# Performance work log

Measured on AMD Instinct MI355X. Metric: run time of the kernel, lower is better.

## Reference

```python
import math
import jax, jax.numpy as jnp
import numpy as np

Bn, NA, NE = 16384, 15, 16
H, NH, DH = 256, 4, 64
DO, DA, DE = 30, 32, 32
NACT, BS = 6, 2048


def setup_inputs():
    key = jax.random.key(0)
    c = [0]
    def nxt():
        c[0] += 1
        return jax.random.fold_in(key, c[0])
    def nrm(shape, scale=1.0):
        return jax.random.normal(nxt(), shape, jnp.float32) * scale
    sH = 1.0 / math.sqrt(H)
    own_raw = nrm((Bn, 1, DO))
    ally_raw = nrm((Bn, NA, DA))
    enemy_raw = nrm((Bn, NE, DE))
    # zero-rows encode invisible entities (mask is derived from all-zero check)
    mA = jax.random.bernoulli(nxt(), 0.8, (Bn, NA)).at[:, 0].set(True)
    mE = jax.random.bernoulli(nxt(), 0.8, (Bn, NE)).at[:, 0].set(True)
    ally_raw = ally_raw * mA[..., None]
    enemy_raw = enemy_raw * mE[..., None]
    return dict(
        own_raw=own_raw, ally_raw=ally_raw, enemy_raw=enemy_raw,
        hidden_state=nrm((Bn, H), 0.1),
        W_own=nrm((H, DO), 1.0 / math.sqrt(DO)), b_own=jnp.zeros((H,)),
        W_ally=nrm((H, DA), 1.0 / math.sqrt(DA)), b_ally=jnp.zeros((H,)),
        W_enemy=nrm((H, DE), 1.0 / math.sqrt(DE)), b_enemy=jnp.zeros((H,)),
        gt_w=nrm((2,), 0.1), gt_b=jnp.zeros((2,)),
        attnA_W=nrm((4, H, H), sH), attnA_b=jnp.zeros((4, H)),
        attnE_W=nrm((4, H, H), sH), attnE_b=jnp.zeros((4, H)),
        clnA_W=nrm((2, H, H), 0.1 * sH), clnA_b=jnp.zeros((2, H)),
        clnE_W=nrm((2, H, H), 0.1 * sH), clnE_b=jnp.zeros((2, H)),
        ln3_g=jnp.ones((3 * H,)), ln3_b=jnp.zeros((3 * H,)),
        gru_Wih=nrm((3 * H, 3 * H), 1.0 / math.sqrt(3 * H)),
        gru_Whh=nrm((3 * H, H), sH),
        gru_bih=jnp.zeros((3 * H,)), gru_bhh=jnp.zeros((3 * H,)),
        Wv_head=nrm((1, H), sH), bv_head=jnp.zeros((1,)),
        Wtb=nrm((2, H), sH), btb=jnp.zeros((2,)),
        log_tau=jnp.zeros((2,)),
        Wmq=nrm((H, H), sH), bmq=jnp.zeros((H,)),
        prototypes=nrm((NACT, H), sH),
        Wqs=nrm((H, H), sH), bqs=jnp.zeros((H,)),
        Wke=nrm((H, H), sH), bke=jnp.zeros((H,)),
        bs=BS,
    )


def _group_temp(cnt, w, b):
    # GroupTemp: positive temperature from group cardinality
    return jax.nn.softplus(w * jnp.log1p(cnt) + b) + 1.0


def _mhga(q, K, mask, temp, W, b):
    # multi-head group attention: single query over a small entity set
    B, N, _ = K.shape
    qh = (q @ W[0].T + b[0]).reshape(B, NH, DH)
    kh = (K @ W[1].T + b[1]).reshape(B, N, NH, DH)
    vh = (K @ W[2].T + b[2]).reshape(B, N, NH, DH)
    s = jnp.einsum('bhd,bnhd->bhn', qh, kh) / math.sqrt(DH)
    s = s / temp[:, None, None]
    s = jnp.where(mask[:, None, :], s, -1e30)
    p = jax.nn.softmax(s, axis=-1)
    z = jnp.einsum('bhn,bnhd->bhd', p, vh).reshape(B, H)
    return z @ W[3].T + b[3]


def _cln(x, cond, W, b, eps=1e-5):
    # conditional LayerNorm: scale/shift predicted from own-feature embedding
    mu = x.mean(-1, keepdims=True)
    var = ((x - mu) ** 2).mean(-1, keepdims=True)
    xn = (x - mu) * jax.lax.rsqrt(var + eps)
    gamma = 1.0 + cond @ W[0].T + b[0]
    beta = cond @ W[1].T + b[1]
    return gamma * xn + beta


def _ln(x, g, b, eps=1e-5):
    mu = x.mean(-1, keepdims=True)
    var = ((x - mu) ** 2).mean(-1, keepdims=True)
    return (x - mu) * jax.lax.rsqrt(var + eps) * g + b


def reference(own_raw, ally_raw, enemy_raw, hidden_state, W_own, b_own,
              W_ally, b_ally, W_enemy, b_enemy, gt_w, gt_b,
              attnA_W, attnA_b, attnE_W, attnE_b,
              clnA_W, clnA_b, clnE_W, clnE_b, ln3_g, ln3_b,
              gru_Wih, gru_Whh, gru_bih, gru_bhh,
              Wv_head, bv_head, Wtb, btb, log_tau,
              Wmq, bmq, prototypes, Wqs, bqs, Wke, bke, bs):
    ally_mask = jnp.any(ally_raw != 0, axis=-1)     # [B,nA]
    enemy_mask = jnp.any(enemy_raw != 0, axis=-1)   # [B,nE]
    e_own = own_raw @ W_own.T + b_own               # [B,1,H]
    A = ally_raw @ W_ally.T + b_ally                # [B,nA,H]
    E = enemy_raw @ W_enemy.T + b_enemy             # [B,nE,H]
    q_src = e_own[:, 0]
    tA = _group_temp(ally_mask.sum(-1).astype(jnp.float32), gt_w[0], gt_b[0])
    tE = _group_temp(enemy_mask.sum(-1).astype(jnp.float32), gt_w[1], gt_b[1])
    zA = _cln(_mhga(q_src, A, ally_mask, tA, attnA_W, attnA_b), q_src, clnA_W, clnA_b)
    zE = _cln(_mhga(q_src, E, enemy_mask, tE, attnE_W, attnE_b), q_src, clnE_W, clnE_b)
    u = _ln(jnp.concatenate([q_src, zA, zE], axis=-1), ln3_g, ln3_b)
    # GRUCell (PyTorch gate layout: r, z, n)
    gi = u @ gru_Wih.T + gru_bih
    gh = hidden_state @ gru_Whh.T + gru_bhh
    ir, iz, inn = jnp.split(gi, 3, axis=-1)
    hr, hz, hn = jnp.split(gh, 3, axis=-1)
    r = jax.nn.sigmoid(ir + hr)
    zg = jax.nn.sigmoid(iz + hz)
    n = jnp.tanh(inn + r * hn)
    h = (1.0 - zg) * n + zg * hidden_state
    V = h @ Wv_head.T + bv_head                     # [B,1]
    tb = h @ Wtb.T + btb
    b_move, b_shoot = tb[:, 0:1], tb[:, 1:2]
    tau_move = jnp.exp(log_tau[0]) + 1e-6
    tau_shoot = jnp.exp(log_tau[1]) + 1e-6
    # prototype movement head
    q_mv = h @ Wmq.T + bmq
    A_move = q_mv @ prototypes.T / math.sqrt(H)
    A_move = A_move - A_move.mean(-1, keepdims=True)
    Q_move = V + b_move + A_move / tau_move
    # shoot pointer head over enemies
    q_sh = h @ Wqs.T + bqs
    Ke = E @ Wke.T + bke
    a = jnp.einsum('bh,bnh->bn', q_sh, Ke) / math.sqrt(H)
    emf = enemy_mask.astype(a.dtype)
    den = jnp.maximum(emf.sum(1, keepdims=True), 1.0)
    a = a - (a * emf).sum(1, keepdims=True) / den
    a = jnp.where(enemy_mask, a, -1e30)
    Q_shoot = V + b_shoot + a / tau_shoot
    Q = jnp.concatenate([Q_move, Q_shoot], axis=-1)[:, None, :]  # [B,1,NACT+nE]
    return Q, h.reshape(bs, -1, H)
```

## Files before the change

kernel.cpp:

```cpp
#include <hip/hip_runtime.h>
#include <math.h>

#define BN 16384

typedef float f32x4 __attribute__((ext_vector_type(4)));
typedef short bf16x8v __attribute__((ext_vector_type(8)));
typedef unsigned short u16x8 __attribute__((ext_vector_type(8)));
typedef unsigned short u16x4 __attribute__((ext_vector_type(4)));

static __device__ inline unsigned short f2bf(float f) {
  unsigned u = __float_as_uint(f);
  return (unsigned short)((u + 0x8000u) >> 16);
}
static __device__ inline float bf2f(unsigned short u) {
  return __uint_as_float(((unsigned)u) << 16);
}

#define XS(r) (((r) >> 1) & 3)

#define WKA_OFF   0
#define WVA_OFF   8192
#define WKE_OFF   16384
#define WVE_OFF   24576
#define WKEF_OFF  32768
#define BKA_OFF   40960
#define BVA_OFF   41216
#define BKE_OFF   41472
#define BVE_OFF   41728
#define BKEF_OFF  41984
#define WMP_OFF   43008
#define BMP_OFF   44544
#define G_OFF     45056
#define BG_OFF    53248
#define WQB_OFF   53312
#define SC0_OFF   53568
#define BMG_OFF   53632
#define CLB_OFF   53888
#define BPJA_OFF  57088
#define BPJE_OFF  57344
#define BGRU_OFF  57600
#define BHD_OFF   16384

#define QSRC_OFF  65536
#define BUF1_OFF  (QSRC_OFF + BN*256)
#define BUF2_OFF  (BUF1_OFF + BN*256)
#define BUF3_OFF  (BUF2_OFF + BN*256)
#define BUF4_OFF  (BUF3_OFF + BN*256)
#define BUF5_OFF  (BUF4_OFF + BN*256)

#define GBUF_OFF  BUF1_OFF
#define AOUTA_OFF BUF3_OFF
#define AOUTE_OFF BUF4_OFF
#define GBB_OFF   BUF5_OFF
#define UB_OFF    (BUF5_OFF + 8388608)

#define HOFF      (BN*22)

#define MGB_S 0
#define CLA_S 65536
#define CLE_S 196608
#define PJA_S 327680
#define PJE_S 360448

__global__ __launch_bounds__(256) void k_fuseA(
    const float* __restrict__ attnA_W, const float* __restrict__ attnA_b,
    const float* __restrict__ attnE_W, const float* __restrict__ attnE_b,
    const float* __restrict__ W_ally,  const float* __restrict__ b_ally,
    const float* __restrict__ W_enemy, const float* __restrict__ b_enemy,
    const float* __restrict__ Wke,     const float* __restrict__ bke,
    const float* __restrict__ clnA_W,  const float* __restrict__ clnE_W,
    float* __restrict__ FW, unsigned short* __restrict__ WBc) {
  int g = blockIdx.x * 256 + threadIdx.x;
  if (g < 81920) {
    int u = g >> 1, t = g & 1;
    int m = u >> 13;
    int r = u & 8191;
    int d = r >> 5, j = r & 31;
    const float *Wout, *Win, *bin, *bout; float *dst, *dstb;
    switch (m) {
      case 0: Wout = attnA_W + 65536;  Win = W_ally;  bin = b_ally;  bout = attnA_b + 256; dst = FW + WKA_OFF;  dstb = FW + BKA_OFF;  break;
      case 1: Wout = attnA_W + 131072; Win = W_ally;  bin = b_ally;  bout = attnA_b + 512; dst = FW + WVA_OFF;  dstb = FW + BVA_OFF;  break;
      case 2: Wout = attnE_W + 65536;  Win = W_enemy; bin = b_enemy; bout = attnE_b + 256; dst = FW + WKE_OFF;  dstb = FW + BKE_OFF;  break;
      case 3: Wout = attnE_W + 131072; Win = W_enemy; bin = b_enemy; bout = attnE_b + 512; dst = FW + WVE_OFF;  dstb = FW + BVE_OFF;  break;
      default:Wout = Wke;              Win = W_enemy; bin = b_enemy; bout = bke;           dst = FW + WKEF_OFF; dstb = FW + BKEF_OFF; break;
    }
    const int c0 = t * 128;
    float acc = 0.f;
    for (int c = c0; c < c0 + 128; ++c) acc += Wout[d*256 + c] * Win[c*32 + j];
    acc += __shfl_xor(acc, 1);
    if (t == 0) dst[d*32 + j] = acc;
    if (j == 0) {
      float b = 0.f;
      for (int c = c0; c < c0 + 128; ++c) b += Wout[d*256 + c] * bin[c];
      b += __shfl_xor(b, 1);
      if (t == 0) dstb[d] = b + bout[d];
    }
  } else {
    int t = g - 81920;
    if (t < 65536) {
      int e = t * 4;
      const float* src = (e < 131072) ? clnA_W : clnE_W;
      int off = (e < 131072) ? 0 : 131072;
      float4 v = *(const float4*)(src + (e - off));
      u16x4 b; b.x = f2bf(v.x); b.y = f2bf(v.y); b.z = f2bf(v.z); b.w = f2bf(v.w);
      *(u16x4*)&WBc[CLA_S + e] = b;
    }
  }
}

__global__ __launch_bounds__(256) void k_fuseB(
    const float* __restrict__ protos, const float* __restrict__ Wmq,
    const float* __restrict__ bmq,    const float* __restrict__ Wqs,
    const float* __restrict__ bqs,
    const float* __restrict__ attnA_W, const float* __restrict__ attnA_b,
    const float* __restrict__ attnE_W, const float* __restrict__ attnE_b,
    const float* __restrict__ clnA_b,  const float* __restrict__ clnE_b,
    float* __restrict__ FW, unsigned short* __restrict__ WBc) {
  int g = blockIdx.x * 256 + threadIdx.x;
  const float* WKe_f = FW + WKEF_OFF;
  const float* bKe_f = FW + BKEF_OFF;
  if (g < 20480) {
    int u = g >> 1, tt = g & 1;
    const int c0 = tt * 128;
    if (u < 1536) {
      int i = u >> 8, c = u & 255;
      float acc = 0.f;
      for (int d = c0; d < c0 + 128; ++d) acc += protos[i*256 + d] * Wmq[d*256 + c];
      acc += __shfl_xor(acc, 1);
      if (tt == 0) FW[WMP_OFF + i*256 + c] = acc;
    } else if (u < 9728) {
      int r = u - 1536;
      int j = r >> 8, c = r & 255;
      float acc = 0.f;
      for (int d = c0; d < c0 + 128; ++d) acc += WKe_f[d*32 + j] * Wqs[d*256 + c];
      acc += __shfl_xor(acc, 1);
      if (tt == 0) FW[G_OFF + j*256 + c] = acc;
    } else if (u < 9984) {
      int c = u - 9728;
      float acc = 0.f;
      for (int d = c0; d < c0 + 128; ++d) acc += Wqs[d*256 + c] * bKe_f[d];
      acc += __shfl_xor(acc, 1);
      if (tt == 0) FW[WQB_OFF + c] = acc;
    } else if (u < 9990) {
      int i = u - 9984;
      float acc = 0.f;
      for (int d = c0; d < c0 + 128; ++d) acc += protos[i*256 + d] * bmq[d];
      acc += __shfl_xor(acc, 1);
      if (tt == 0) FW[BMP_OFF + i] = acc;
    } else if (u < 10022) {
      int j = u - 9990;
      float acc = 0.f;
      for (int d = c0; d < c0 + 128; ++d) acc += WKe_f[d*32 + j] * bqs[d];
      acc += __shfl_xor(acc, 1);
      if (tt == 0) FW[BG_OFF + j] = acc;
    } else if (u == 10022) {
      float acc = 0.f;
      for (int d = c0; d < c0 + 128; ++d) acc += bqs[d] * bKe_f[d];
      acc += __shfl_xor(acc, 1);
      if (tt == 0) FW[SC0_OFF] = acc;
    }
  } else if (g < 87296) {
    int t = g - 20480;
    if (t < 65536) {
      int r = t >> 8, c = t & 255;
      int br = r >> 7, jj = r & 127, h = jj >> 5, jc = jj & 31;
      const float* W0 = br ? attnE_W : attnA_W;
      const float* Wk = FW + (br ? WKE_OFF : WKA_OFF);
      float acc = 0.f;
      for (int d = 0; d < 64; ++d)
        acc += W0[(h*64+d)*256 + c] * Wk[(h*64+d)*32 + jc];
      WBc[MGB_S + r*256 + c] = f2bf(acc);
    } else if (t < 65792) {
      int r = t - 65536;
      int br = r >> 7, jj = r & 127, h = jj >> 5, jc = jj & 31;
      const float* b0 = br ? attnE_b : attnA_b;
      const float* Wk = FW + (br ? WKE_OFF : WKA_OFF);
      float acc = 0.f;
      for (int d = 0; d < 64; ++d) acc += b0[h*64+d] * Wk[(h*64+d)*32 + jc];
      FW[BMG_OFF + r] = acc;
    } else {
      int c = t - 65792;
      FW[CLB_OFF + c] = (c < 512) ? clnA_b[c] : clnE_b[c - 512];
    }
  } else {
    int t = g - 87296;
    if (t < 65536) {
      int br = t >> 15;
      int r0 = t & 32767;
      int o = r0 >> 7, r = r0 & 127, h = r >> 5, j = r & 31;
      const float* Wp = (br ? attnE_W : attnA_W) + 196608;
      const float* Wv = FW + (br ? WVE_OFF : WVA_OFF);
      float acc = 0.f;
      for (int d = 0; d < 64; ++d)
        acc += Wp[o*256 + h*64 + d] * Wv[(h*64+d)*32 + j];
      WBc[(br ? PJE_S : PJA_S) + o*128 + r] = f2bf(acc);
    } else if (t < 66048) {
      int r0 = t - 65536;
      int br = r0 >> 8, c = r0 & 255;
      const float* Wp = (br ? attnE_W : attnA_W) + 196608;
      const float* bv = FW + (br ? BVE_OFF : BVA_OFF);
      const float* pb = (br ? attnE_b : attnA_b) + 768;
      float acc = pb[c];
      for (int d = 0; d < 256; ++d) acc += Wp[c*256 + d] * bv[d];
      FW[(br ? BPJE_OFF : BPJA_OFF) + c] = acc;
    }
  }
}

__global__ __launch_bounds__(256) void k_fuse4(
    const float* __restrict__ Wv_head, const float* __restrict__ bv_head,
    const float* __restrict__ Wtb, const float* __restrict__ btb,
    float* __restrict__ FW, unsigned short* __restrict__ WHD) {
  int g = blockIdx.x * 256 + threadIdx.x;
  if (g < 32768) {
    int r = g >> 8, c = g & 255;
    float v;
    if (r == 0)       v = Wv_head[c];
    else if (r == 1)  v = Wtb[c];
    else if (r == 2)  v = Wtb[256 + c];
    else if (r < 9)   v = FW[WMP_OFF + (r - 3) * 256 + c];
    else if (r < 41)  v = FW[G_OFF + (r - 9) * 256 + c];
    else if (r == 41) v = FW[WQB_OFF + c];
    else              v = 0.f;
    WHD[r * 256 + c] = f2bf(v);
  } else if (g < 32896) {
    int r = g - 32768;
    float v;
    if (r == 0)       v = bv_head[0];
    else if (r == 1)  v = btb[0];
    else if (r == 2)  v = btb[1];
    else if (r < 9)   v = FW[BMP_OFF + r - 3];
    else if (r < 41)  v = FW[BG_OFF + r - 9];
    else if (r == 41) v = FW[SC0_OFF];
    else              v = 0.f;
    FW[BHD_OFF + r] = v;
  }
}

__global__ __launch_bounds__(256) void k_gruw2(
    const float* __restrict__ Wih, const float* __restrict__ Whh,
    const float* __restrict__ bih, const float* __restrict__ bhh,
    unsigned short* __restrict__ WF, float* __restrict__ BG) {
  int t = blockIdx.x * 256 + threadIdx.x;
  if (t < 131072) {
    int l = t & 63;
    int n = (t >> 6) & 3;
    int cq = (t >> 8) & 3;
    int bx = (t >> 10) & 3;
    int ch = t >> 12;
    int lr = l & 15, lk = l >> 4;
    int d = bx * 64 + cq * 16 + lr;
    int kb = ch * 32 + lk * 8;
    float fa[8];
    bool zero = (kb < 768) ? (n == 3) : (n == 2);
    if (zero) {
      #pragma unroll
      for (int i = 0; i < 8; ++i) fa[i] = 0.f;
    } else if (kb < 768) {
      const float* src = Wih + (long)(n * 256 + d) * 768 + kb;
      *(float4*)&fa[0] = *(const float4*)(src);
      *(float4*)&fa[4] = *(const float4*)(src + 4);
    } else {
      int rh = (n == 3 ? 512 : n * 256) + d;
      const float* src = Whh + (long)rh * 256 + (kb - 768);
      *(float4*)&fa[0] = *(const float4*)(src);
      *(float4*)&fa[4] = *(const float4*)(src + 4);
    }
    u16x8 pk;
    #pragma unroll
    for (int i = 0; i < 8; ++i) pk[i] = f2bf(fa[i]);
    *(u16x8*)&WF[(long)t * 8] = pk;
  } else if (t < 132096) {
    int p = t - 131072;
    int X = p >> 8, df = (p >> 6) & 3, g = (p >> 4) & 3, i = p & 15;
    int d = X * 64 + df * 16 + i;
    float v;
    if (g == 0)      v = bih[d] + bhh[d];
    else if (g == 1) v = bih[256 + d] + bhh[256 + d];
    else if (g == 2) v = bih[512 + d];
    else             v = bhh[512 + d];
    BG[p] = v;
  }
}

template<int K, int NOUT>
__global__ __launch_bounds__(256) void k_densek(
    const float* __restrict__ A, const float* __restrict__ W,
    const float* __restrict__ bias, unsigned short* __restrict__ Cb) {
  constexpr int KB = 32;
  __shared__ float As[64][36];
  const int tid = threadIdx.x;
  const int s0 = blockIdx.x * 64;
  const int o0 = blockIdx.y * 64;
  const int ox = (tid & 15) * 4;
  const int sy = (tid >> 4) * 4;
  float acc[4][4] = {};
  const float* Abase = A + (long)s0 * K;
  for (int idx = tid; idx < 64 * KB; idx += 256) {
    int s = idx >> 5, c = idx & 31;
    As[s][c] = (c < K) ? Abase[(long)s * K + c] : 0.f;
  }
  __syncthreads();
  for (int kk = 0; kk < KB; kk += 4) {
    float a4[4][4];
    #pragma unroll
    for (int sj = 0; sj < 4; ++sj)
      *(float4*)a4[sj] = *(const float4*)&As[sy + sj][kk];
    #pragma unroll
    for (int oi = 0; oi < 4; ++oi) {
      float w4[4];
      #pragma unroll
      for (int kx = 0; kx < 4; ++kx) {
        int k = kk + kx;
        w4[kx] = (k < K) ? W[(long)(o0 + ox + oi) * K + k] : 0.f;
      }
      #pragma unroll
      for (int sj = 0; sj < 4; ++sj)
        #pragma unroll
        for (int kx = 0; kx < 4; ++kx)
          acc[sj][oi] = fmaf(a4[sj][kx], w4[kx], acc[sj][oi]);
    }
  }
  #pragma unroll
  for (int sj = 0; sj < 4; ++sj) {
    u16x4 b4;
    b4.x = f2bf(acc[sj][0] + bias[o0 + ox + 0]);
    b4.y = f2bf(acc[sj][1] + bias[o0 + ox + 1]);
    b4.z = f2bf(acc[sj][2] + bias[o0 + ox + 2]);
    b4.w = f2bf(acc[sj][3] + bias[o0 + ox + 3]);
    *(u16x4*)&Cb[(long)(s0 + sy + sj) * NOUT + o0 + ox] = b4;
  }
}

#define MM_PROLOG(GDX)                                                        \
  __shared__ __align__(16) unsigned short As[4096];                           \
  __shared__ __align__(16) unsigned short Ws[4096];                           \
  const int tid = threadIdx.x;                                                \
  const int pid = blockIdx.y * (GDX) + blockIdx.x;                            \
  const int bx = (pid >> 3) % (GDX);                                          \
  const int by = ((pid >> 3) / (GDX)) * 8 + (pid & 7);                        \
  const long s0 = (long)by * 128;                                             \
  const int wv = tid >> 6, l = tid & 63;                                      \
  const int wm = (wv >> 1) * 64, wn = (wv & 1) * 64;                          \
  const int lr = l & 15, lk = l >> 4;                                         \
  const int wrow = tid >> 2;                                                  \
  const int wslot = tid & 3;                                                  \
  (void)wrow; (void)wslot;                                                    \
  f32x4 acc[4][4] = {};

#define MM_MFMA_STEP                                                          \
  {                                                                           \
    bf16x8v af[4], bw[4];                                                     \
    _Pragma("unroll")                                                         \
    for (int m = 0; m < 4; ++m) {                                             \
      const int r = wm + m * 16 + lr;                                         \
      af[m] = *(const bf16x8v*)&As[r * 32 + ((lk ^ XS(r)) * 8)];              \
    }                                                                         \
    _Pragma("unroll")                                                         \
    for (int n = 0; n < 4; ++n) {                                             \
      const int r = wn + n * 16 + lr;                                         \
      bw[n] = *(const bf16x8v*)&Ws[r * 32 + ((lk ^ XS(r)) * 8)];              \
    }                                                                         \
    _Pragma("unroll")                                                         \
    for (int m = 0; m < 4; ++m)                                               \
      _Pragma("unroll")                                                       \
      for (int n = 0; n < 4; ++n)                                             \
        acc[m][n] = __builtin_amdgcn_mfma_f32_16x16x32_bf16(af[m], bw[n], acc[m][n], 0, 0, 0); \
  }

__global__ __launch_bounds__(256) void k_mm_qs(
    const unsigned short* __restrict__ Abf, const unsigned short* __restrict__ W,
    const float* __restrict__ bias, unsigned short* __restrict__ Cg,
    unsigned short* __restrict__ Cgb) {
  MM_PROLOG(10)
  const int o0 = bx * 128;
  u16x8 pw[2], pa_b[2];
  const unsigned short* Wb = W + (long)o0 * 256;
  #pragma unroll
  for (int p = 0; p < 2; ++p) {
    const int r = wrow + 64 * p;
    pw[p]   = *(const u16x8*)(Wb + (long)r * 256 + wslot * 8);
    pa_b[p] = *(const u16x8*)(Abf + (s0 + r) * 256 + wslot * 8);
  }
  for (int ch = 0; ch < 8; ++ch) {
    if (ch) __syncthreads();
    #pragma unroll
    for (int p = 0; p < 2; ++p) {
      const int r = wrow + 64 * p;
      const int ps = (wslot ^ XS(r)) * 8;
      *(u16x8*)&Ws[r * 32 + ps] = pw[p];
      *(u16x8*)&As[r * 32 + ps] = pa_b[p];
    }
    __syncthreads();
    if (ch + 1 < 8) {
      const int k0 = (ch + 1) * 32;
      #pragma unroll
      for (int p = 0; p < 2; ++p) {
        const int r = wrow + 64 * p;
        pw[p]   = *(const u16x8*)(Wb + (long)r * 256 + k0 + wslot * 8);
        pa_b[p] = *(const u16x8*)(Abf + (s0 + r) * 256 + k0 + wslot * 8);
      }
    }
    MM_MFMA_STEP
  }
  if (bx < 2) {
    const int ob = bx * 128;
    #pragma unroll
    for (int n = 0; n < 4; ++n) {
      const float b = bias[o0 + wn + n * 16 + lr];
      #pragma unroll
      for (int m = 0; m < 4; ++m) {
        const long rowb = s0 + wm + m * 16 + lk * 4;
        #pragma unroll
        for (int r = 0; r < 4; ++r)
          Cg[(rowb + r) * 256 + ob + wn + n * 16 + lr] = f2bf(acc[m][n][r] + b);
      }
    }
  } else {
    const int ob = (bx - 2) * 128;
    #pragma unroll
    for (int n = 0; n < 4; ++n) {
      const float b = bias[o0 + wn + n * 16 + lr];
      #pragma unroll
      for (int m = 0; m < 4; ++m) {
        const long rowb = s0 + wm + m * 16 + lk * 4;
        #pragma unroll
        for (int r = 0; r < 4; ++r)
          Cgb[(rowb + r) * 1024 + ob + wn + n * 16 + lr] = f2bf(acc[m][n][r] + b);
      }
    }
  }
}

__global__ __launch_bounds__(256) void k_mm_pv(
    const unsigned short* __restrict__ pal, const unsigned short* __restrict__ W,
    const float* __restrict__ bias, unsigned short* __restrict__ CA,
    unsigned short* __restrict__ CE) {
  MM_PROLOG(4)
  const int o0 = bx * 128;
  const int br = bx >> 1;
  const unsigned short* Abf = pal + br * 128;
  u16x8 pw[2], pa_b[2];
  const unsigned short* Wb = W + (long)o0 * 128;
  #pragma unroll
  for (int p = 0; p < 2; ++p) {
    const int r = wrow + 64 * p;
    pw[p]   = *(const u16x8*)(Wb + (long)r * 128 + wslot * 8);
    pa_b[p] = *(const u16x8*)(Abf + (s0 + r) * 256 + wslot * 8);
  }
  for (int ch = 0; ch < 4; ++ch) {
    if (ch) __syncthreads();
    #pragma unroll
    for (int p = 0; p < 2; ++p) {
      const int r = wrow + 64 * p;
      const int ps = (wslot ^ XS(r)) * 8;
      *(u16x8*)&Ws[r * 32 + ps] = pw[p];
      *(u16x8*)&As[r * 32 + ps] = pa_b[p];
    }
    __syncthreads();
    if (ch + 1 < 4) {
      const int k0 = (ch + 1) * 32;
      #pragma unroll
      for (int p = 0; p < 2; ++p) {
        const int r = wrow + 64 * p;
        pw[p]   = *(const u16x8*)(Wb + (long)r * 128 + k0 + wslot * 8);
        pa_b[p] = *(const u16x8*)(Abf + (s0 + r) * 256 + k0 + wslot * 8);
      }
    }
    MM_MFMA_STEP
  }
  unsigned short* C = br ? CE : CA;
  const int ob = (bx & 1) * 128;
  #pragma unroll
  for (int n = 0; n < 4; ++n) {
    const float b = bias[o0 + wn + n * 16 + lr];
    #pragma unroll
    for (int m = 0; m < 4; ++m) {
      const long rowb = s0 + wm + m * 16 + lk * 4;
      #pragma unroll
      for (int r = 0; r < 4; ++r)
        C[(rowb + r) * 256 + ob + wn + n * 16 + lr] = f2bf(acc[m][n][r] + b);
    }
  }
}

__global__ __launch_bounds__(512, 4) void k_gru8(
    const unsigned short* __restrict__ UB, const float* __restrict__ hid,
    const unsigned short* __restrict__ WF, const float* __restrict__ BG,
    float* __restrict__ hout) {
  __shared__ __align__(16) unsigned short As[2][4096];
  const int tid = threadIdx.x;
  const int pid = blockIdx.y * 4 + blockIdx.x;
  const int lin = pid >> 3;
  const int bx = lin & 3;
  const int by = (lin >> 2) * 8 + (pid & 7);
  const long s0 = (long)by * 128;
  const int wv = tid >> 6, l = tid & 63;
  const int sh = wv >> 2;
  const int cq = wv & 3;
  const int lr = l & 15, lk = l >> 4;
  const int row = tid >> 2;
  const int q = tid & 3;

  f32x4 acc[4][4] = {};
  u16x8 bwc0, bwc1, bwc2, bwn0, bwn1, bwn2;
  u16x8 pa_b;
  float4 pa_f[2];

  const unsigned short* WFb = WF + (((long)bx * 4 + cq) * 4) * 512 + l * 8;
#define WFRAG(CH, N) (*(const u16x8*)(WFb + ((long)(CH) * 64 + (N)) * 512))

#define GRU8_MFMA(G0, G1, G2)                                                 \
  {                                                                           \
    const unsigned short* AsC = As[cur];                                      \
    bf16x8v af[4];                                                            \
    _Pragma("unroll")                                                         \
    for (int m = 0; m < 4; ++m) {                                             \
      const int r = sh * 64 + m * 16 + lr;                                    \
      af[m] = *(const bf16x8v*)&AsC[r * 32 + ((lk ^ XS(r)) * 8)];             \
    }                                                                         \
    _Pragma("unroll")                                                         \
    for (int m = 0; m < 4; ++m) {                                             \
      acc[m][G0] = __builtin_amdgcn_mfma_f32_16x16x32_bf16(af[m], (bf16x8v)bwc0, acc[m][G0], 0, 0, 0); \
      acc[m][G1] = __builtin_amdgcn_mfma_f32_16x16x32_bf16(af[m], (bf16x8v)bwc1, acc[m][G1], 0, 0, 0); \
      acc[m][G2] = __builtin_amdgcn_mfma_f32_16x16x32_bf16(af[m], (bf16x8v)bwc2, acc[m][G2], 0, 0, 0); \
    }                                                                         \
  }

  pa_b = *(const u16x8*)(UB + (s0 + row) * 768 + q * 8);
  *(u16x8*)&As[0][row * 32 + ((q ^ XS(row)) * 8)] = pa_b;
  bwc0 = WFRAG(0, 0); bwc1 = WFRAG(0, 1); bwc2 = WFRAG(0, 2);
  __syncthreads();

  for (int ch = 0; ch < 24; ++ch) {
    const int cur = ch & 1;
    const int k0 = (ch + 1) * 32;
    if (ch + 1 < 24) {
      pa_b = *(const u16x8*)(UB + (s0 + row) * 768 + k0 + q * 8);
      bwn0 = WFRAG(ch + 1, 0); bwn1 = WFRAG(ch + 1, 1); bwn2 = WFRAG(ch + 1, 2);
    } else {
      const float* Af = hid + (s0 + row) * 256 + q * 8;
      pa_f[0] = *(const float4*)(Af);
      pa_f[1] = *(const float4*)(Af + 4);
      bwn0 = WFRAG(24, 0); bwn1 = WFRAG(24, 1); bwn2 = WFRAG(24, 3);
    }
    GRU8_MFMA(0, 1, 2)
    if (ch + 1 < 24) {
      *(u16x8*)&As[cur ^ 1][row * 32 + ((q ^ XS(row)) * 8)] = pa_b;
    } else {
      float fa[8];
      *(float4*)&fa[0] = pa_f[0];
      *(float4*)&fa[4] = pa_f[1];
      u16x8 pk;
      #pragma unroll
      for (int i = 0; i < 8; ++i) pk[i] = f2bf(fa[i]);
      *(u16x8*)&As[cur ^ 1][row * 32 + ((q ^ XS(row)) * 8)] = pk;
    }
    __syncthreads();
    bwc0 = bwn0; bwc1 = bwn1; bwc2 = bwn2;
  }
  for (int ch = 24; ch < 32; ++ch) {
    const int cur = ch & 1;
    if (ch + 1 < 32) {
      const int k0 = (ch + 1) * 32;
      const int km = k0 - 768;
      const float* Af = hid + (s0 + row) * 256 + km + q * 8;
      pa_f[0] = *(const float4*)(Af);
      pa_f[1] = *(const float4*)(Af + 4);
      bwn0 = WFRAG(ch + 1, 0); bwn1 = WFRAG(ch + 1, 1); bwn2 = WFRAG(ch + 1, 3);
    }
    GRU8_MFMA(0, 1, 3)
    if (ch + 1 < 32) {
      float fa[8];
      *(float4*)&fa[0] = pa_f[0];
      *(float4*)&fa[4] = pa_f[1];
      u16x8 pk;
      #pragma unroll
      for (int i = 0; i < 8; ++i) pk[i] = f2bf(fa[i]);
      *(u16x8*)&As[cur ^ 1][row * 32 + ((q ^ XS(row)) * 8)] = pk;
      __syncthreads();
      bwc0 = bwn0; bwc1 = bwn1; bwc2 = bwn2;
    }
  }

  const int d = bx * 64 + cq * 16 + lr;
  const int bb = bx * 256 + cq * 64 + lr;
  const float bR  = BG[bb];
  const float bZ  = BG[bb + 16];
  const float bNi = BG[bb + 32];
  const float bNh = BG[bb + 48];
  #pragma unroll
  for (int m = 0; m < 4; ++m) {
    const long srow = s0 + sh * 64 + m * 16 + lk * 4;
    #pragma unroll
    for (int rr = 0; rr < 4; ++rr) {
      const long s = srow + rr;
      const float r_ = 1.f / (1.f + expf(-(acc[m][0][rr] + bR)));
      const float z_ = 1.f / (1.f + expf(-(acc[m][1][rr] + bZ)));
      const float n_ = tanhf(acc[m][2][rr] + bNi + r_ * (acc[m][3][rr] + bNh));
      const float hp = hid[s * 256 + d];
      hout[s * 256 + d] = (1.f - z_) * n_ + z_ * hp;
    }
  }
#undef GRU8_MFMA
#undef WFRAG
}

__global__ __launch_bounds__(256) void k_core2(
    const float* __restrict__ rawA, const float* __restrict__ rawE,
    const unsigned short* __restrict__ g, const float* __restrict__ gt_w,
    const float* __restrict__ gt_b, unsigned short* __restrict__ pal) {
  __shared__ float A_[4][15][36];
  __shared__ float E_[4][16][36];
  __shared__ float G_[4][8][32];
  __shared__ float P_[4][8][16];
  const int tid = threadIdx.x;
  const int w = tid >> 6, l = tid & 63;
  const long s = (long)blockIdx.x * 4 + w;

  const float* ra = rawA + s * 480;
  const float* re = rawE + s * 512;
  const unsigned short* gr = g + s * 256;
  #pragma unroll
  for (int i = l; i < 120; i += 64) {
    float4 v = *(const float4*)(ra + i * 4);
    *(float4*)&A_[w][i >> 3][(i & 7) * 4] = v;
  }
  #pragma unroll
  for (int i = l; i < 128; i += 64) {
    float4 v = *(const float4*)(re + i * 4);
    *(float4*)&E_[w][i >> 3][(i & 7) * 4] = v;
  }
  {
    u16x4 v = *(const u16x4*)(gr + l * 4);
    float4 f = { bf2f(v.x), bf2f(v.y), bf2f(v.z), bf2f(v.w) };
    *(float4*)&G_[w][l >> 3][(l & 7) * 4] = f;
  }
  __syncthreads();

  bool mv = false;
  if (l < 15) {
    #pragma unroll
    for (int c = 0; c < 8; ++c) {
      float4 x = *(const float4*)&A_[w][l][c * 4];
      mv |= (x.x != 0.f) | (x.y != 0.f) | (x.z != 0.f) | (x.w != 0.f);
    }
  } else if (l >= 16 && l < 32) {
    #pragma unroll
    for (int c = 0; c < 8; ++c) {
      float4 x = *(const float4*)&E_[w][l - 16][c * 4];
      mv |= (x.x != 0.f) | (x.y != 0.f) | (x.z != 0.f) | (x.w != 0.f);
    }
  }
  unsigned long long bal = __ballot(mv);
  unsigned mA = (unsigned)bal & 0x7FFFu;
  unsigned mE = (unsigned)(bal >> 16) & 0xFFFFu;
  float xa = gt_w[0] * log1pf((float)__popc(mA)) + gt_b[0];
  float spa = fmaxf(xa, 0.f) + log1pf(expf(-fabsf(xa)));
  float scaleA = 1.f / (8.f * (spa + 1.f));
  float xe = gt_w[1] * log1pf((float)__popc(mE)) + gt_b[1];
  float spe = fmaxf(xe, 0.f) + log1pf(expf(-fabsf(xe)));
  float scaleE = 1.f / (8.f * (spe + 1.f));

  {
    const int h = l >> 4, n = l & 15;
    const bool okA = (n < 15) && ((mA >> n) & 1);
    const bool okE = (mE >> n) & 1;
    const float* arow = &A_[w][n < 15 ? n : 0][0];
    const float* erow = &E_[w][n][0];
    const float* garow = &G_[w][h][0];
    const float* gerow = &G_[w][4 + h][0];
    float accA = 0.f, accE = 0.f;
    #pragma unroll
    for (int j = 0; j < 32; ++j) {
      accA = fmaf(garow[j], arow[j], accA);
      accE = fmaf(gerow[j], erow[j], accE);
    }
    float sA = okA ? accA * scaleA : -INFINITY;
    float sE = okE ? accE * scaleE : -INFINITY;
    float mAx = sA, mEx = sE;
    #pragma unroll
    for (int off = 8; off; off >>= 1) {
      mAx = fmaxf(mAx, __shfl_xor(mAx, off));
      mEx = fmaxf(mEx, __shfl_xor(mEx, off));
    }
    float eA = okA ? expf(sA - mAx) : 0.f;
    float eE = okE ? expf(sE - mEx) : 0.f;
    float suA = eA, suE = eE;
    #pragma unroll
    for (int off = 8; off; off >>= 1) {
      suA += __shfl_xor(suA, off);
      suE += __shfl_xor(suE, off);
    }
    P_[w][h][n] = eA / suA;
    P_[w][4 + h][n] = eE / suE;
  }
  __syncthreads();

  {
    const int j = l & 31, hh = l >> 5;
    unsigned short* po = pal + s * 256 + hh * 32 + j;
    #pragma unroll
    for (int r = 0; r < 2; ++r) {
      const int ha = r * 2 + hh;
      float a0 = 0.f, a1 = 0.f;
      #pragma unroll
      for (int n = 0; n < 15; ++n)
        a0 = fmaf(P_[w][ha][n], A_[w][n][j], a0);
      #pragma unroll
      for (int n = 0; n < 16; ++n)
        a1 = fmaf(P_[w][4 + ha][n], E_[w][n][j], a1);
      po[r * 64] = f2bf(a0);
      po[128 + r * 64] = f2bf(a1);
    }
  }
}

__global__ __launch_bounds__(256) void k_clnln(
    const unsigned short* __restrict__ aA, const unsigned short* __restrict__ aE,
    const unsigned short* __restrict__ qsb, const unsigned short* __restrict__ gbb,
    const float* __restrict__ g, const float* __restrict__ b,
    unsigned short* __restrict__ UB) {
  int w = threadIdx.x >> 6, l = threadIdx.x & 63;
  long s = (long)blockIdx.x * 4 + w;
  int d = l * 4;
  u16x4 av = *(const u16x4*)(aA + s * 256 + d);
  u16x4 ev = *(const u16x4*)(aE + s * 256 + d);
  u16x4 qv = *(const u16x4*)(qsb + s * 256 + d);
  float4 vA = { bf2f(av.x), bf2f(av.y), bf2f(av.z), bf2f(av.w) };
  float4 vE = { bf2f(ev.x), bf2f(ev.y), bf2f(ev.z), bf2f(ev.w) };
  float4 vq = { bf2f(qv.x), bf2f(qv.y), bf2f(qv.z), bf2f(qv.w) };
  const unsigned short* gbr = gbb + s * 1024;
  float sumA = vA.x + vA.y + vA.z + vA.w;
  float ssqA = vA.x*vA.x + vA.y*vA.y + vA.z*vA.z + vA.w*vA.w;
  float sumE = vE.x + vE.y + vE.z + vE.w;
  float ssqE = vE.x*vE.x + vE.y*vE.y + vE.z*vE.z + vE.w*vE.w;
  #pragma unroll
  for (int off = 32; off > 0; off >>= 1) {
    sumA += __shfl_xor(sumA, off); ssqA += __shfl_xor(ssqA, off);
    sumE += __shfl_xor(sumE, off); ssqE += __shfl_xor(ssqE, off);
  }
  float muA = sumA * (1.f / 256.f);
  float rstdA = rsqrtf(ssqA * (1.f / 256.f) - muA * muA + 1e-5f);
  float muE = sumE * (1.f / 256.f);
  float rstdE = rsqrtf(ssqE * (1.f / 256.f) - muE * muE + 1e-5f);

  u16x4 u0 = *(const u16x4*)(gbr + d);
  u16x4 u1 = *(const u16x4*)(gbr + 256 + d);
  u16x4 u2 = *(const u16x4*)(gbr + 512 + d);
  u16x4 u3 = *(const u16x4*)(gbr + 768 + d);
  float4 gA4 = { bf2f(u0.x), bf2f(u0.y), bf2f(u0.z), bf2f(u0.w) };
  float4 bA4 = { bf2f(u1.x), bf2f(u1.y), bf2f(u1.z), bf2f(u1.w) };
  float4 gE4 = { bf2f(u2.x), bf2f(u2.y), bf2f(u2.z), bf2f(u2.w) };
  float4 bE4 = { bf2f(u3.x), bf2f(u3.y), bf2f(u3.z), bf2f(u3.w) };
  float4 zA, zE;
  zA.x = (1.f + gA4.x) * ((vA.x - muA) * rstdA) + bA4.x;
  zA.y = (1.f + gA4.y) * ((vA.y - muA) * rstdA) + bA4.y;
  zA.z = (1.f + gA4.z) * ((vA.z - muA) * rstdA) + bA4.z;
  zA.w = (1.f + gA4.w) * ((vA.w - muA) * rstdA) + bA4.w;
  zE.x = (1.f + gE4.x) * ((vE.x - muE) * rstdE) + bE4.x;
  zE.y = (1.f + gE4.y) * ((vE.y - muE) * rstdE) + bE4.y;
  zE.z = (1.f + gE4.z) * ((vE.z - muE) * rstdE) + bE4.z;
  zE.w = (1.f + gE4.w) * ((vE.w - muE) * rstdE) + bE4.w;

  float sum = vq.x+vq.y+vq.z+vq.w + zA.x+zA.y+zA.z+zA.w + zE.x+zE.y+zE.z+zE.w;
  float ssq = vq.x*vq.x+vq.y*vq.y+vq.z*vq.z+vq.w*vq.w
            + zA.x*zA.x+zA.y*zA.y+zA.z*zA.z+zA.w*zA.w
            + zE.x*zE.x+zE.y*zE.y+zE.z*zE.z+zE.w*zE.w;
  #pragma unroll
  for (int off = 32; off > 0; off >>= 1) {
    sum += __shfl_xor(sum, off); ssq += __shfl_xor(ssq, off);
  }
  float mu = sum * (1.f / 768.f);
  float rstd = rsqrtf(ssq * (1.f / 768.f) - mu * mu + 1e-5f);

  float4 g0 = *(const float4*)(g + d),       b0 = *(const float4*)(b + d);
  float4 g1 = *(const float4*)(g + 256 + d), b1 = *(const float4*)(b + 256 + d);
  float4 g2 = *(const float4*)(g + 512 + d), b2 = *(const float4*)(b + 512 + d);
  unsigned short* ur = UB + s * 768;
  u16x4 o;
  o.x = f2bf((vq.x - mu) * rstd * g0.x + b0.x);
  o.y = f2bf((vq.y - mu) * rstd * g0.y + b0.y);
  o.z = f2bf((vq.z - mu) * rstd * g0.z + b0.z);
  o.w = f2bf((vq.w - mu) * rstd * g0.w + b0.w);
  *(u16x4*)&ur[d] = o;
  o.x = f2bf((zA.x - mu) * rstd * g1.x + b1.x);
  o.y = f2bf((zA.y - mu) * rstd * g1.y + b1.y);
  o.z = f2bf((zA.z - mu) * rstd * g1.z + b1.z);
  o.w = f2bf((zA.w - mu) * rstd * g1.w + b1.w);
  *(u16x4*)&ur[256 + d] = o;
  o.x = f2bf((zE.x - mu) * rstd * g2.x + b2.x);
  o.y = f2bf((zE.y - mu) * rstd * g2.y + b2.y);
  o.z = f2bf((zE.z - mu) * rstd * g2.z + b2.z);
  o.w = f2bf((zE.w - mu) * rstd * g2.w + b2.w);
  *(u16x4*)&ur[512 + d] = o;
}

__global__ __launch_bounds__(256) void k_headsmm(
    const float* __restrict__ h, const unsigned short* __restrict__ WHD,
    const float* __restrict__ BHD, const float* __restrict__ eraw,
    const float* __restrict__ log_tau, float* __restrict__ Qout) {
  __shared__ __align__(16) unsigned short As[2048];
  __shared__ __align__(16) unsigned short Ws[2048];
  __shared__ float obs[64][49];
  const int tid = threadIdx.x;
  const long s0 = (long)blockIdx.x * 64;
  const int wv = tid >> 6, l = tid & 63;
  const int lr = l & 15, lk = l >> 4;
  const int row = tid >> 2;
  const int q = tid & 3;
  f32x4 acc[4] = {};
  u16x8 pw;
  float4 pa_f[2];
  pw = *(const u16x8*)(WHD + (long)row * 256 + q * 8);
  {
    const float* Af = h + (s0 + row) * 256 + q * 8;
    pa_f[0] = *(const float4*)(Af);
    pa_f[1] = *(const float4*)(Af + 4);
  }
  for (int ch = 0; ch < 8; ++ch) {
    if (ch) __syncthreads();
    *(u16x8*)&Ws[row * 32 + ((q ^ XS(row)) * 8)] = pw;
    {
      float fa[8];
      *(float4*)&fa[0] = pa_f[0];
      *(float4*)&fa[4] = pa_f[1];
      u16x8 pk;
      #pragma unroll
      for (int i = 0; i < 8; ++i) pk[i] = f2bf(fa[i]);
      *(u16x8*)&As[row * 32 + ((q ^ XS(row)) * 8)] = pk;
    }
    __syncthreads();
    if (ch + 1 < 8) {
      const int k0 = (ch + 1) * 32;
      pw = *(const u16x8*)(WHD + (long)row * 256 + k0 + q * 8);
      const float* Af = h + (s0 + row) * 256 + k0 + q * 8;
      pa_f[0] = *(const float4*)(Af);
      pa_f[1] = *(const float4*)(Af + 4);
    }
    {
      bf16x8v af, bw[4];
      {
        const int r = wv * 16 + lr;
        af = *(const bf16x8v*)&As[r * 32 + ((lk ^ XS(r)) * 8)];
      }
      #pragma unroll
      for (int n = 0; n < 4; ++n) {
        const int r = n * 16 + lr;
        bw[n] = *(const bf16x8v*)&Ws[r * 32 + ((lk ^ XS(r)) * 8)];
      }
      #pragma unroll
      for (int n = 0; n < 4; ++n)
        acc[n] = __builtin_amdgcn_mfma_f32_16x16x32_bf16(af, bw[n], acc[n], 0, 0, 0);
    }
  }
  #pragma unroll
  for (int n = 0; n < 3; ++n) {
    const int col = n * 16 + lr;
    const float b = BHD[col];
    const int rowo = wv * 16 + lk * 4;
    #pragma unroll
    for (int rr = 0; rr < 4; ++rr)
      obs[rowo + rr][col] = acc[n][rr] + b;
  }
  __syncthreads();
  const float itm = 1.f / (expf(log_tau[0]) + 1e-6f);
  const float its = 1.f / (expf(log_tau[1]) + 1e-6f);
  for (int rep = 0; rep < 4; ++rep) {
    const int sloc = rep * 16 + (tid >> 4);
    const int i = tid & 15;
    const long s = s0 + sloc;
    const float V = obs[sloc][0];
    const float* er = eraw + s * 512 + i * 32;
    bool valid = false; float a0 = 0.f;
    #pragma unroll
    for (int jb = 0; jb < 8; ++jb) {
      float4 e4 = *(const float4*)(er + jb * 4);
      valid |= (e4.x != 0.f) | (e4.y != 0.f) | (e4.z != 0.f) | (e4.w != 0.f);
      a0 += obs[sloc][9 + jb * 4 + 0] * e4.x + obs[sloc][9 + jb * 4 + 1] * e4.y +
            obs[sloc][9 + jb * 4 + 2] * e4.z + obs[sloc][9 + jb * 4 + 3] * e4.w;
    }
    float a = (a0 + obs[sloc][41]) * 0.0625f;
    float sa = valid ? a : 0.f;
    float cv = valid ? 1.f : 0.f;
    #pragma unroll
    for (int off = 8; off > 0; off >>= 1) {
      sa += __shfl_xor(sa, off);
      cv += __shfl_xor(cv, off);
    }
    float me = sa / fmaxf(cv, 1.f);
    Qout[s * 22 + 6 + i] = V + obs[sloc][2] + (valid ? (a - me) * its : -1e30f * its);
    if (i < 6) {
      float mean = 0.f;
      #pragma unroll
      for (int t = 0; t < 6; ++t) mean += obs[sloc][3 + t];
      mean *= (1.f / 6.f);
      Qout[s * 22 + i] = V + obs[sloc][1] + (obs[sloc][3 + i] - mean) * 0.0625f * itm;
    }
  }
}

extern "C" void kernel_launch(void* const* d_in, const int* in_sizes, int n_in,
                              void* d_out, int out_size, void* d_ws, size_t ws_size,
                              hipStream_t stream) {
  const float* own_raw   = (const float*)d_in[0];
  const float* ally_raw  = (const float*)d_in[1];
  const float* enemy_raw = (const float*)d_in[2];
  const float* hidden    = (const float*)d_in[3];
  const float* W_own     = (const float*)d_in[4];
  const float* b_own     = (const float*)d_in[5];
  const float* W_ally    = (const float*)d_in[6];
  const float* b_ally    = (const float*)d_in[7];
  const float* W_enemy   = (const float*)d_in[8];
  const float* b_enemy   = (const float*)d_in[9];
  const float* gt_w      = (const float*)d_in[10];
  const float* gt_b      = (const float*)d_in[11];
  const float* attnA_W   = (const float*)d_in[12];
  const float* attnA_b   = (const float*)d_in[13];
  const float* attnE_W   = (const float*)d_in[14];
  const float* attnE_b   = (const float*)d_in[15];
  const float* clnA_W    = (const float*)d_in[16];
  const float* clnA_b    = (const float*)d_in[17];
  const float* clnE_W    = (const float*)d_in[18];
  const float* clnE_b    = (const float*)d_in[19];
  const float* ln3_g     = (const float*)d_in[20];
  const float* ln3_b     = (const float*)d_in[21];
  const float* gru_Wih   = (const float*)d_in[22];
  const float* gru_Whh   = (const float*)d_in[23];
  const float* gru_bih   = (const float*)d_in[24];
  const float* gru_bhh   = (const float*)d_in[25];
  const float* Wv_head   = (const float*)d_in[26];
  const float* bv_head   = (const float*)d_in[27];
  const float* Wtb       = (const float*)d_in[28];
  const float* btb       = (const float*)d_in[29];
  const float* log_tau   = (const float*)d_in[30];
  const float* Wmq       = (const float*)d_in[31];
  const float* bmq       = (const float*)d_in[32];
  const float* protos    = (const float*)d_in[33];
  const float* Wqs       = (const float*)d_in[34];
  const float* bqs       = (const float*)d_in[35];
  const float* Wke       = (const float*)d_in[36];
  const float* bke       = (const float*)d_in[37];

  float* ws  = (float*)d_ws;
  float* out = (float*)d_out;
  float* hout = out + HOFF;
  unsigned short* WB   = (unsigned short*)hout;
  unsigned short* qsb  = (unsigned short*)(ws + BUF2_OFF);
  unsigned short* palb = (unsigned short*)(ws + QSRC_OFF);
  unsigned short* WHD  = (unsigned short*)ws;
  unsigned short* wfrag = (unsigned short*)(ws + BUF1_OFF);
  unsigned short* gb16 = (unsigned short*)(ws + GBUF_OFF);
  unsigned short* aoA  = (unsigned short*)(ws + AOUTA_OFF);
  unsigned short* aoE  = (unsigned short*)(ws + AOUTE_OFF);
  unsigned short* gbb  = (unsigned short*)(ws + GBB_OFF);
  unsigned short* ub   = (unsigned short*)(ws + UB_OFF);

  k_fuseA<<<576, 256, 0, stream>>>(attnA_W, attnA_b, attnE_W, attnE_b,
                                   W_ally, b_ally, W_enemy, b_enemy, Wke, bke,
                                   clnA_W, clnE_W, ws, WB);
  k_fuseB<<<599, 256, 0, stream>>>(protos, Wmq, bmq, Wqs, bqs,
                                   attnA_W, attnA_b, attnE_W, attnE_b,
                                   clnA_b, clnE_b, ws, WB);
  k_fuse4<<<129, 256, 0, stream>>>(Wv_head, bv_head, Wtb, btb, ws, WHD);

  k_densek<30, 256><<<dim3(BN/64, 4), 256, 0, stream>>>(own_raw, W_own, b_own, qsb);

  k_mm_qs<<<dim3(10, 128), 256, 0, stream>>>(qsb, WB, ws + BMG_OFF, gb16, gbb);

  k_core2<<<BN/4, 256, 0, stream>>>(ally_raw, enemy_raw, gb16, gt_w, gt_b, palb);

  k_gruw2<<<516, 256, 0, stream>>>(gru_Wih, gru_Whh, gru_bih, gru_bhh,
                                   wfrag, ws + BGRU_OFF);

  k_mm_pv<<<dim3(4, 128), 256, 0, stream>>>(palb, WB + PJA_S, ws + BPJA_OFF,
                                            aoA, aoE);

  k_clnln<<<BN/4, 256, 0, stream>>>(aoA, aoE, qsb, gbb, ln3_g, ln3_b, ub);

  k_gru8<<<dim3(4, 128), 512, 0, stream>>>(ub, hidden, wfrag, ws + BGRU_OFF, hout);

  k_headsmm<<<BN/64, 256, 0, stream>>>(hout, WHD, ws + BHD_OFF, enemy_raw,
                                       log_tau, out);
}
```

Before: 174.1 us.

## Store GRU input in MFMA fragment layout and load operands directly from global

k_clnln now writes the layer-normed GRU input in a pre-swizzled MFMA A-fragment layout. The GRU kernel then loads A fragments straight from global memory into registers instead of staging them through a double-buffered LDS tile with barriers. This removes LDS traffic and __syncthreads, at the cost of losing explicit software prefetch of the next chunk. It also relies on the memory system to hide latency, since occupancy hints were loosened. The hidden-state part is still read as fp32 from global and converted per fragment, with some redundant reads across waves.

New measurement: 209.5 us. +20.3%, slower.

```diff
diff --git a/kernel.cpp b/kernel.cpp
--- a/kernel.cpp
+++ b/kernel.cpp
@@ -484,11 +484,10 @@
   }
 }
 
-__global__ __launch_bounds__(512, 4) void k_gru8(
-    const unsigned short* __restrict__ UB, const float* __restrict__ hid,
+__global__ __launch_bounds__(512) void k_gru9(
+    const unsigned short* __restrict__ UFR, const float* __restrict__ hid,
     const unsigned short* __restrict__ WF, const float* __restrict__ BG,
     float* __restrict__ hout) {
-  __shared__ __align__(16) unsigned short As[2][4096];
   const int tid = threadIdx.x;
   const int pid = blockIdx.y * 4 + blockIdx.x;
   const int lin = pid >> 3;
@@ -499,87 +498,48 @@
   const int sh = wv >> 2;
   const int cq = wv & 3;
   const int lr = l & 15, lk = l >> 4;
-  const int row = tid >> 2;
-  const int q = tid & 3;
 
   f32x4 acc[4][4] = {};
-  u16x8 bwc0, bwc1, bwc2, bwn0, bwn1, bwn2;
-  u16x8 pa_b;
-  float4 pa_f[2];
 
   const unsigned short* WFb = WF + (((long)bx * 4 + cq) * 4) * 512 + l * 8;
-#define WFRAG(CH, N) (*(const u16x8*)(WFb + ((long)(CH) * 64 + (N)) * 512))
-
-#define GRU8_MFMA(G0, G1, G2)                                                 \
-  {                                                                           \
-    const unsigned short* AsC = As[cur];                                      \
-    bf16x8v af[4];                                                            \
-    _Pragma("unroll")                                                         \
-    for (int m = 0; m < 4; ++m) {                                             \
-      const int r = sh * 64 + m * 16 + lr;                                    \
-      af[m] = *(const bf16x8v*)&AsC[r * 32 + ((lk ^ XS(r)) * 8)];             \
-    }                                                                         \
-    _Pragma("unroll")                                                         \
-    for (int m = 0; m < 4; ++m) {                                             \
-      acc[m][G0] = __builtin_amdgcn_mfma_f32_16x16x32_bf16(af[m], (bf16x8v)bwc0, acc[m][G0], 0, 0, 0); \
-      acc[m][G1] = __builtin_amdgcn_mfma_f32_16x16x32_bf16(af[m], (bf16x8v)bwc1, acc[m][G1], 0, 0, 0); \
-      acc[m][G2] = __builtin_amdgcn_mfma_f32_16x16x32_bf16(af[m], (bf16x8v)bwc2, acc[m][G2], 0, 0, 0); \
-    }                                                                         \
-  }
-
-  pa_b = *(const u16x8*)(UB + (s0 + row) * 768 + q * 8);
-  *(u16x8*)&As[0][row * 32 + ((q ^ XS(row)) * 8)] = pa_b;
-  bwc0 = WFRAG(0, 0); bwc1 = WFRAG(0, 1); bwc2 = WFRAG(0, 2);
-  __syncthreads();
+  const unsigned short* AFb = UFR + (((long)by * 32) * 8 + sh * 4) * 512 + (long)l * 8;
 
   for (int ch = 0; ch < 24; ++ch) {
-    const int cur = ch & 1;
-    const int k0 = (ch + 1) * 32;
-    if (ch + 1 < 24) {
-      pa_b = *(const u16x8*)(UB + (s0 + row) * 768 + k0 + q * 8);
-      bwn0 = WFRAG(ch + 1, 0); bwn1 = WFRAG(ch + 1, 1); bwn2 = WFRAG(ch + 1, 2);
-    } else {
-      const float* Af = hid + (s0 + row) * 256 + q * 8;
-      pa_f[0] = *(const float4*)(Af);
-      pa_f[1] = *(const float4*)(Af + 4);
-      bwn0 = WFRAG(24, 0); bwn1 = WFRAG(24, 1); bwn2 = WFRAG(24, 3);
-    }
-    GRU8_MFMA(0, 1, 2)
-    if (ch + 1 < 24) {
-      *(u16x8*)&As[cur ^ 1][row * 32 + ((q ^ XS(row)) * 8)] = pa_b;
-    } else {
-      float fa[8];
-      *(float4*)&fa[0] = pa_f[0];
-      *(float4*)&fa[4] = pa_f[1];
+    bf16x8v af[4];
+    #pragma unroll
+    for (int m = 0; m < 4; ++m)
+      af[m] = *(const bf16x8v*)(AFb + ((long)ch * 8 + m) * 512);
+    bf16x8v b0 = *(const bf16x8v*)(WFb + ((long)ch * 64 + 0) * 512);
+    bf16x8v b1 = *(const bf16x8v*)(WFb + ((long)ch * 64 + 1) * 512);
+    bf16x8v b2 = *(const bf16x8v*)(WFb + ((long)ch * 64 + 2) * 512);
+    #pragma unroll
+    for (int m = 0; m < 4; ++m) {
+      acc[m][0] = __builtin_amdgcn_mfma_f32_16x16x32_bf16(af[m], b0, acc[m][0], 0, 0, 0);
+      acc[m][1] = __builtin_amdgcn_mfma_f32_16x16x32_bf16(af[m], b1, acc[m][1], 0, 0, 0);
+      acc[m][2] = __builtin_amdgcn_mfma_f32_16x16x32_bf16(af[m], b2, acc[m][2], 0, 0, 0);
+    }
+  }
+  for (int ch = 24; ch < 32; ++ch) {
+    const int km = (ch - 24) * 32 + lk * 8;
+    bf16x8v af[4];
+    #pragma unroll
+    for (int m = 0; m < 4; ++m) {
+      const float* Af = hid + (s0 + sh * 64 + m * 16 + lr) * 256 + km;
+      float4 v0 = *(const float4*)(Af);
+      float4 v1 = *(const float4*)(Af + 4);
       u16x8 pk;
-      #pragma unroll
-      for (int i = 0; i < 8; ++i) pk[i] = f2bf(fa[i]);
-      *(u16x8*)&As[cur ^ 1][row * 32 + ((q ^ XS(row)) * 8)] = pk;
-    }
-    __syncthreads();
-    bwc0 = bwn0; bwc1 = bwn1; bwc2 = bwn2;
-  }
-  for (int ch = 24; ch < 32; ++ch) {
-    const int cur = ch & 1;
-    if (ch + 1 < 32) {
-      const int k0 = (ch + 1) * 32;
-      const int km = k0 - 768;
-      const float* Af = hid + (s0 + row) * 256 + km + q * 8;
-      pa_f[0] = *(const float4*)(Af);
-      pa_f[1] = *(const float4*)(Af + 4);
-      bwn0 = WFRAG(ch + 1, 0); bwn1 = WFRAG(ch + 1, 1); bwn2 = WFRAG(ch + 1, 3);
-    }
-    GRU8_MFMA(0, 1, 3)
-    if (ch + 1 < 32) {
-      float fa[8];
-      *(float4*)&fa[0] = pa_f[0];
-      *(float4*)&fa[4] = pa_f[1];
-      u16x8 pk;
-      #pragma unroll
-      for (int i = 0; i < 8; ++i) pk[i] = f2bf(fa[i]);
-      *(u16x8*)&As[cur ^ 1][row * 32 + ((q ^ XS(row)) * 8)] = pk;
-      __syncthreads();
-      bwc0 = bwn0; bwc1 = bwn1; bwc2 = bwn2;
+      pk[0] = f2bf(v0.x); pk[1] = f2bf(v0.y); pk[2] = f2bf(v0.z); pk[3] = f2bf(v0.w);
+      pk[4] = f2bf(v1.x); pk[5] = f2bf(v1.y); pk[6] = f2bf(v1.z); pk[7] = f2bf(v1.w);
+      af[m] = (bf16x8v)pk;
+    }
+    bf16x8v b0 = *(const bf16x8v*)(WFb + ((long)ch * 64 + 0) * 512);
+    bf16x8v b1 = *(const bf16x8v*)(WFb + ((long)ch * 64 + 1) * 512);
+    bf16x8v b3 = *(const bf16x8v*)(WFb + ((long)ch * 64 + 3) * 512);
+    #pragma unroll
+    for (int m = 0; m < 4; ++m) {
+      acc[m][0] = __builtin_amdgcn_mfma_f32_16x16x32_bf16(af[m], b0, acc[m][0], 0, 0, 0);
+      acc[m][1] = __builtin_amdgcn_mfma_f32_16x16x32_bf16(af[m], b1, acc[m][1], 0, 0, 0);
+      acc[m][3] = __builtin_amdgcn_mfma_f32_16x16x32_bf16(af[m], b3, acc[m][3], 0, 0, 0);
     }
   }
 
@@ -602,8 +562,6 @@
       hout[s * 256 + d] = (1.f - z_) * n_ + z_ * hp;
     }
   }
-#undef GRU8_MFMA
-#undef WFRAG
 }
 
 __global__ __launch_bounds__(256) void k_core2(
@@ -720,7 +678,7 @@
     const unsigned short* __restrict__ aA, const unsigned short* __restrict__ aE,
     const unsigned short* __restrict__ qsb, const unsigned short* __restrict__ gbb,
     const float* __restrict__ g, const float* __restrict__ b,
-    unsigned short* __restrict__ UB) {
+    unsigned short* __restrict__ UFR) {
   int w = threadIdx.x >> 6, l = threadIdx.x & 63;
   long s = (long)blockIdx.x * 4 + w;
   int d = l * 4;
@@ -777,23 +735,38 @@
   float4 g0 = *(const float4*)(g + d),       b0 = *(const float4*)(b + d);
   float4 g1 = *(const float4*)(g + 256 + d), b1 = *(const float4*)(b + 256 + d);
   float4 g2 = *(const float4*)(g + 512 + d), b2 = *(const float4*)(b + 512 + d);
-  unsigned short* ur = UB + s * 768;
+
+  const long ub0 = (long)(s >> 7) * 32;
+  const int mf = (s >> 4) & 7;
+  const int lrr = s & 15;
   u16x4 o;
   o.x = f2bf((vq.x - mu) * rstd * g0.x + b0.x);
   o.y = f2bf((vq.y - mu) * rstd * g0.y + b0.y);
   o.z = f2bf((vq.z - mu) * rstd * g0.z + b0.z);
   o.w = f2bf((vq.w - mu) * rstd * g0.w + b0.w);
-  *(u16x4*)&ur[d] = o;
+  {
+    int k0 = d;
+    long addr = ((ub0 + (k0 >> 5)) * 8 + mf) * 512 + ((((k0 >> 3) & 3) * 16 + lrr) * 8) + (k0 & 7);
+    *(u16x4*)&UFR[addr] = o;
+  }
   o.x = f2bf((zA.x - mu) * rstd * g1.x + b1.x);
   o.y = f2bf((zA.y - mu) * rstd * g1.y + b1.y);
   o.z = f2bf((zA.z - mu) * rstd * g1.z + b1.z);
   o.w = f2bf((zA.w - mu) * rstd * g1.w + b1.w);
-  *(u16x4*)&ur[256 + d] = o;
+  {
+    int k0 = 256 + d;
+    long addr = ((ub0 + (k0 >> 5)) * 8 + mf) * 512 + ((((k0 >> 3) & 3) * 16 + lrr) * 8) + (k0 & 7);
+    *(u16x4*)&UFR[addr] = o;
+  }
   o.x = f2bf((zE.x - mu) * rstd * g2.x + b2.x);
   o.y = f2bf((zE.y - mu) * rstd * g2.y + b2.y);
   o.z = f2bf((zE.z - mu) * rstd * g2.z + b2.z);
   o.w = f2bf((zE.w - mu) * rstd * g2.w + b2.w);
-  *(u16x4*)&ur[512 + d] = o;
+  {
+    int k0 = 512 + d;
+    long addr = ((ub0 + (k0 >> 5)) * 8 + mf) * 512 + ((((k0 >> 3) & 3) * 16 + lrr) * 8) + (k0 & 7);
+    *(u16x4*)&UFR[addr] = o;
+  }
 }
 
 __global__ __launch_bounds__(256) void k_headsmm(
@@ -954,7 +927,7 @@
   unsigned short* aoA  = (unsigned short*)(ws + AOUTA_OFF);
   unsigned short* aoE  = (unsigned short*)(ws + AOUTE_OFF);
   unsigned short* gbb  = (unsigned short*)(ws + GBB_OFF);
-  unsigned short* ub   = (unsigned short*)(ws + UB_OFF);
+  unsigned short* ufr  = (unsigned short*)(ws + UB_OFF);
 
   k_fuseA<<<576, 256, 0, stream>>>(attnA_W, attnA_b, attnE_W, attnE_b,
                                    W_ally, b_ally, W_enemy, b_enemy, Wke, bke,
@@ -976,9 +949,9 @@
   k_mm_pv<<<dim3(4, 128), 256, 0, stream>>>(palb, WB + PJA_S, ws + BPJA_OFF,
                                             aoA, aoE);
 
-  k_clnln<<<BN/4, 256, 0, stream>>>(aoA, aoE, qsb, gbb, ln3_g, ln3_b, ub);
-
-  k_gru8<<<dim3(4, 128), 512, 0, stream>>>(ub, hidden, wfrag, ws + BGRU_OFF, hout);
+  k_clnln<<<BN/4, 256, 0, stream>>>(aoA, aoE, qsb, gbb, ln3_g, ln3_b, ufr);
+
+  k_gru9<<<dim3(4, 128), 512, 0, stream>>>(ufr, hidden, wfrag, ws + BGRU_OFF, hout);
 
   k_headsmm<<<BN/64, 256, 0, stream>>>(hout, WHD, ws + BHD_OFF, enemy_raw,
                                        log_tau, out);
```
